# Performance work log

Hardware: AMD Instinct MI355X
Metric: run time of the kernel (lower is better)

Reference implementation:

```python
import jax, jax.numpy as jnp
import numpy as np

NUM_CAPSULE = 128   # must equal steps (seq_len) for the reshape in the original code
DIM_CAPSULE = 64
ROUTINGS = 3
EPS = 1e-7          # K.epsilon()


def pos_emb(x):
    """Sinusoidal position embedding added to x over its last two dims [..., S, D].
    Matches the Keras code: evens use sin(pos/10000^(2k/D)), odds use cos with the
    same frequency (odds-1 == 2k), interleaved via stack+reshape."""
    S, D = x.shape[-2], x.shape[-1]
    pos = jnp.arange(S, dtype=x.dtype)[:, None]                      # [S,1]
    inv_freq = 1.0 / jnp.power(10000.0, (2.0 * jnp.arange(D // 2, dtype=x.dtype)) / D)
    ang = pos * inv_freq[None, :]                                    # [S, D/2]
    pe = jnp.stack([jnp.sin(ang), jnp.cos(ang)], axis=-1).reshape(S, D)
    return x + pe


def squash(s):
    ss = jnp.sum(s * s, axis=-1, keepdims=True)
    scale = ss / (1.0 + ss) / jnp.sqrt(ss + EPS)
    return scale * s


def setup_inputs() -> dict:
    key = jax.random.key(0)
    k1, k2 = jax.random.split(key)
    B, steps, in_dim = 32, 128, 256
    u_vecs = jax.random.normal(k1, (B, steps, in_dim), dtype=jnp.float32)
    mask = jnp.ones((B, steps), dtype=jnp.float32)
    # glorot_uniform for capsule kernel (1, in_dim, dim_capsule)
    lim = float(np.sqrt(6.0 / (in_dim + DIM_CAPSULE)))
    W = jax.random.uniform(k2, (1, in_dim, DIM_CAPSULE), jnp.float32, -lim, lim)
    return {"u_vecs": u_vecs, "mask": mask, "W": W}


def reference(u_vecs, mask, W):
    B, steps, in_dim = u_vecs.shape
    N, D = NUM_CAPSULE, DIM_CAPSULE  # N == steps by construction
    # share_weights branch: tile W across steps, permute, add PE, flatten to a conv1d
    # kernel of width 1 -> a plain [in_dim, steps*D] projection matrix.
    tmp = jnp.transpose(jnp.broadcast_to(W, (steps, in_dim, D)), (1, 0, 2))  # [in_dim, steps, D]
    kernel = pos_emb(tmp).reshape(in_dim, steps * D)                          # [in_dim, steps*D]
    u_hat = jnp.einsum('bsi,io->bso', u_vecs, kernel)                         # [B, steps, steps*D]
    u_hat = pos_emb(u_hat)
    u_hat = u_hat.reshape(B, steps, N, D).transpose(0, 2, 1, 3)               # [B, N, In, D]
    b = jnp.zeros((B, N, steps), dtype=u_hat.dtype)                           # routing logits
    m = mask[:, None, :]                                                      # [B, 1, In]
    outputs = None
    for i in range(ROUTINGS):
        # softmax over the num_capsule axis (permute->softmax(-1)->permute in Keras)
        c = jax.nn.softmax(b, axis=1) * m                                     # [B, N, In]
        outputs = squash(jnp.einsum('bni,bnid->bnd', c, u_hat))               # [B, N, D]
        if i < ROUTINGS - 1:
            b = jnp.einsum('bnd,bnid->bni', outputs, u_hat)                   # agreement
    return outputs
```

## Files before the change

### kernel.cpp

```cpp
#include <hip/hip_runtime.h>
#include <math.h>

#define NB 32
#define NS 128
#define NI 256
#define NC 128
#define ND 64

#define L4 9.210340371976184f

__global__ __launch_bounds__(256) void k_prep(const float* __restrict__ u,
                                              const float* __restrict__ W,
                                              float* __restrict__ M,
                                              float* __restrict__ U,
                                              float* __restrict__ PE1) {
    int blk = blockIdx.x;
    int t = threadIdx.x;
    if (blk < 1024) {
        __shared__ float us[4][NI];
        int g = t >> 6, lane = t & 63;
        int row = blk * 4 + g;
        float4 v4 = ((const float4*)(u + (size_t)row * NI))[lane];
        ((float4*)us[g])[lane] = v4;
        float rs = v4.x + v4.y + v4.z + v4.w;
#pragma unroll
        for (int o = 32; o > 0; o >>= 1) rs += __shfl_xor(rs, o);
        if (lane == 0) U[row] = rs;
        float acc = 0.f;
#pragma unroll 8
        for (int i = 0; i < NI; ++i)
            acc = fmaf(us[g][i], W[i * ND + lane], acc);
        M[row * ND + lane] = acc;
    } else {
        int idx = (blk - 1024) * 256 + t;
        int n = idx >> 6, d = idx & 63;
        float ang = (float)n * __expf(-L4 * (float)(d >> 1) * (1.f / 32.f));
        float sv, cv;
        __sincosf(ang, &sv, &cv);
        PE1[idx] = (d & 1) ? cv : sv;
    }
}

__global__ __launch_bounds__(256, 4) void kR(const float* __restrict__ M,
                                             const float* __restrict__ U,
                                             const float* __restrict__ PE1,
                                             const float* __restrict__ cg,
                                             const float* __restrict__ mask,
                                             float* __restrict__ og,
                                             float* __restrict__ bl,
                                             int first, int last) {
    int bp = blockIdx.x;
    int n  = bp & 127;
    int b0 = (bp >> 7) * 2;
    int t  = threadIdx.x;

    __shared__ float  cs[NS][2];
    __shared__ float  Us[NS][2];
    __shared__ float4 redw[2][4][16];
    __shared__ float4 outs4[2][16];
    __shared__ float  tpar[2][2];
    __shared__ float  sc2[2][2];
    __shared__ float  red2[2][NS * 17];

    {
        int bh = t >> 7, s = t & 127;
        int b = b0 + bh;
        float uu = U[b * NS + s];
        float cv = first ? mask[b * NS + s] * (1.f / 128.f)
                         : cg[(b * NC + n) * NS + s];
        cs[s][bh] = cv;
        Us[s][bh] = uu;
        float p = cv * uu;
#pragma unroll
        for (int o = 32; o > 0; o >>= 1) p += __shfl_xor(p, o);
        if ((t & 63) == 0) tpar[bh][(t >> 6) & 1] = p;
    }

    float4 p14;
    if (t < 32) p14 = ((const float4*)PE1)[n * 16 + (t & 15)];

    int dq = t & 15, sq = t >> 4;
    int s0 = sq * 8;
    int k2 = n * 32 + dq * 2;
    float g0 = __expf(-L4 * (float)k2 * (1.f / 4096.f));
    float g1 = __expf(-L4 * (float)(k2 + 1) * (1.f / 4096.f));
    float sa = __sinf((float)s0 * g0), ca = __cosf((float)s0 * g0);
    float sb = __sinf((float)s0 * g1), cb = __cosf((float)s0 * g1);
    float sg0 = __sinf(g0), cg0 = __cosf(g0);
    float sg1 = __sinf(g1), cg1 = __cosf(g1);
    __syncthreads();

    float4 cc4[4];
    {
        const float4* csp = (const float4*)&cs[s0][0];
        cc4[0] = csp[0]; cc4[1] = csp[1]; cc4[2] = csp[2]; cc4[3] = csp[3];
    }

    const float4* M4a = (const float4*)(M + (size_t)(b0 * NS) * ND) + dq;
    const float4* M4b = M4a + NS * 16;
    float4 va[8], vb[8];
    float4 acc0 = make_float4(0.f, 0.f, 0.f, 0.f);
    float4 acc1 = make_float4(0.f, 0.f, 0.f, 0.f);
#pragma unroll
    for (int i = 0; i < 8; ++i) {
        int s = s0 + i;
        float4 m0 = M4a[s * 16];
        float4 m1 = M4b[s * 16];
        float2 cc = ((const float2*)cc4)[i];
        float4 u0, u1;
        u0.x = m0.x + sa; u0.y = m0.y + ca; u0.z = m0.z + sb; u0.w = m0.w + cb;
        u1.x = m1.x + sa; u1.y = m1.y + ca; u1.z = m1.z + sb; u1.w = m1.w + cb;
        va[i] = u0; vb[i] = u1;
        acc0.x = fmaf(cc.x, u0.x, acc0.x);
        acc0.y = fmaf(cc.x, u0.y, acc0.y);
        acc0.z = fmaf(cc.x, u0.z, acc0.z);
        acc0.w = fmaf(cc.x, u0.w, acc0.w);
        acc1.x = fmaf(cc.y, u1.x, acc1.x);
        acc1.y = fmaf(cc.y, u1.y, acc1.y);
        acc1.z = fmaf(cc.y, u1.z, acc1.z);
        acc1.w = fmaf(cc.y, u1.w, acc1.w);
        float nsa = fmaf(sa, cg0, ca * sg0);
        float nca = fmaf(ca, cg0, -sa * sg0);
        sa = nsa; ca = nca;
        float nsb = fmaf(sb, cg1, cb * sg1);
        float ncb = fmaf(cb, cg1, -sb * sg1);
        sb = nsb; cb = ncb;
    }
#pragma unroll
    for (int o = 16; o <= 32; o <<= 1) {
        acc0.x += __shfl_xor(acc0.x, o); acc0.y += __shfl_xor(acc0.y, o);
        acc0.z += __shfl_xor(acc0.z, o); acc0.w += __shfl_xor(acc0.w, o);
        acc1.x += __shfl_xor(acc1.x, o); acc1.y += __shfl_xor(acc1.y, o);
        acc1.z += __shfl_xor(acc1.z, o); acc1.w += __shfl_xor(acc1.w, o);
    }
    if ((t & 48) == 0) {
        int w = t >> 6;
        redw[0][w][dq] = acc0;
        redw[1][w][dq] = acc1;
    }
    __syncthreads();

    if (t < 32) {
        int bh = t >> 4, q = t & 15;
        float4 r0 = redw[bh][0][q], r1 = redw[bh][1][q];
        float4 r2 = redw[bh][2][q], r3 = redw[bh][3][q];
        float4 o;
        o.x = r0.x + r1.x + r2.x + r3.x;
        o.y = r0.y + r1.y + r2.y + r3.y;
        o.z = r0.z + r1.z + r2.z + r3.z;
        o.w = r0.w + r1.w + r2.w + r3.w;
        float T2 = tpar[bh][0] + tpar[bh][1];
        o.x = fmaf(p14.x, T2, o.x);
        o.y = fmaf(p14.y, T2, o.y);
        o.z = fmaf(p14.z, T2, o.z);
        o.w = fmaf(p14.w, T2, o.w);
        outs4[bh][q] = o;
        float ssq = o.x * o.x + o.y * o.y + o.z * o.z + o.w * o.w;
        float ppu = o.x * p14.x + o.y * p14.y + o.z * p14.z + o.w * p14.w;
#pragma unroll
        for (int o2 = 1; o2 <= 8; o2 <<= 1) {
            ssq += __shfl_xor(ssq, o2);
            ppu += __shfl_xor(ppu, o2);
        }
        if (q == 0) {
            sc2[bh][0] = ssq / (1.f + ssq) * rsqrtf(ssq + 1e-7f);
            sc2[bh][1] = ppu;
        }
    }
    __syncthreads();

    if (last) {
        if (t < 32) {
            int bh = t >> 4, q = t & 15;
            float sc = sc2[bh][0];
            float4 o = outs4[bh][q];
            o.x *= sc; o.y *= sc; o.z *= sc; o.w *= sc;
            ((float4*)og)[((b0 + bh) * NC + n) * 16 + q] = o;
        }
        return;
    }

    float4 oa = outs4[0][dq], ob = outs4[1][dq];
#pragma unroll
    for (int i = 0; i < 8; ++i) {
        int s = s0 + i;
        float4 v0 = va[i], v1 = vb[i];
        red2[0][s * 17 + dq] = v0.x * oa.x + v0.y * oa.y + v0.z * oa.z + v0.w * oa.w;
        red2[1][s * 17 + dq] = v1.x * ob.x + v1.y * ob.y + v1.z * ob.z + v1.w * ob.w;
    }
    __syncthreads();
    {
        int bh = t >> 7, s = t & 127;
        const float* r = &red2[bh][s * 17];
        float sum = 0.f;
#pragma unroll
        for (int q = 0; q < 16; ++q) sum += r[q];
        bl[((b0 + bh) * NC + n) * NS + s] =
            sc2[bh][0] * (sum + sc2[bh][1] * Us[s][bh]);
    }
}

__global__ __launch_bounds__(256) void kS(const float* __restrict__ bl,
                                          const float* __restrict__ mask,
                                          float* __restrict__ c) {
    int blk = blockIdx.x;
    int b = blk >> 3, s0 = (blk & 7) * 16;
    int t = threadIdx.x;

    __shared__ float tl[NC][17];
    __shared__ float pr[16][17];
    __shared__ float ps[16][17];
    __shared__ float itot[16], msk[16];

    if (t < 16) msk[t] = mask[b * NS + s0 + t];
#pragma unroll
    for (int i = 0; i < 8; ++i) {
        int idx = i * 256 + t;
        int n = idx >> 4, si = idx & 15;
        tl[n][si] = bl[(b * NC + n) * NS + s0 + si];
    }
    __syncthreads();

    int si = t & 15, ch = t >> 4;
    float mx = -1e30f;
#pragma unroll
    for (int j = 0; j < 8; ++j) mx = fmaxf(mx, tl[ch * 8 + j][si]);
    pr[ch][si] = mx;
    __syncthreads();

    mx = pr[0][si];
#pragma unroll
    for (int jc = 1; jc < 16; ++jc) mx = fmaxf(mx, pr[jc][si]);
    float sm = 0.f;
#pragma unroll
    for (int j = 0; j < 8; ++j) {
        float e = __expf(tl[ch * 8 + j][si] - mx);
        tl[ch * 8 + j][si] = e;
        sm += e;
    }
    ps[ch][si] = sm;
    __syncthreads();

    if (t < 16) {
        float tot = 0.f;
#pragma unroll
        for (int jc = 0; jc < 16; ++jc) tot += ps[jc][t];
        itot[t] = msk[t] / tot;
    }
    __syncthreads();

#pragma unroll
    for (int i = 0; i < 8; ++i) {
        int idx = i * 256 + t;
        int n = idx >> 4, sj = idx & 15;
        c[(b * NC + n) * NS + s0 + sj] = tl[n][sj] * itot[sj];
    }
}

extern "C" void kernel_launch(void* const* d_in, const int* in_sizes, int n_in,
                              void* d_out, int out_size, void* d_ws, size_t ws_size,
                              hipStream_t stream) {
    const float* u    = (const float*)d_in[0];
    const float* mask = (const float*)d_in[1];
    const float* W    = (const float*)d_in[2];
    float* out = (float*)d_out;

    float* ws  = (float*)d_ws;
    float* M   = ws;
    float* U   = M + NB * NS * ND;
    float* PE1 = U + NB * NS;
    float* c   = PE1 + NC * ND;
    float* bl  = c + NB * NC * NS;

    k_prep<<<1056, 256, 0, stream>>>(u, W, M, U, PE1);

    kR<<<2048, 256, 0, stream>>>(M, U, PE1, c, mask, out, bl, 1, 0);
    kS<<<NB * 8, 256, 0, stream>>>(bl, mask, c);
    kR<<<2048, 256, 0, stream>>>(M, U, PE1, c, mask, out, bl, 0, 0);
    kS<<<NB * 8, 256, 0, stream>>>(bl, mask, c);
    kR<<<2048, 256, 0, stream>>>(M, U, PE1, c, mask, out, bl, 0, 1);
}
```

Baseline: 103.8 us.

## Process two capsules per routing block and vectorize the projection in prep

The routing kernel now handles two capsules per block, so each M load feeds both capsules and the grid shrinks from 2048 to 1024 blocks. The goal is to halve global reads of M and the per-block setup cost. In exchange each thread holds twice as many register arrays and the block uses more shared memory, with launch bounds lowered to 2 blocks per SM. Separately, the prep kernel's projection splits the input dimension across lane groups, loads W as float4 and reduces partial sums with shuffles.

```diff
diff --git a/kernel.cpp b/kernel.cpp
--- a/kernel.cpp
+++ b/kernel.cpp
@@ -26,11 +26,28 @@
 #pragma unroll
         for (int o = 32; o > 0; o >>= 1) rs += __shfl_xor(rs, o);
         if (lane == 0) U[row] = rs;
-        float acc = 0.f;
+
+        int ih = lane >> 4, dq = lane & 15;
+        int base = ih * 64;
+        const float4* W4 = (const float4*)W;
+        float4 acc = make_float4(0.f, 0.f, 0.f, 0.f);
 #pragma unroll 8
-        for (int i = 0; i < NI; ++i)
-            acc = fmaf(us[g][i], W[i * ND + lane], acc);
-        M[row * ND + lane] = acc;
+        for (int ii = 0; ii < 64; ++ii) {
+            float uu = us[g][base + ii];
+            float4 w4 = W4[(base + ii) * 16 + dq];
+            acc.x = fmaf(uu, w4.x, acc.x);
+            acc.y = fmaf(uu, w4.y, acc.y);
+            acc.z = fmaf(uu, w4.z, acc.z);
+            acc.w = fmaf(uu, w4.w, acc.w);
+        }
+#pragma unroll
+        for (int o = 16; o <= 32; o <<= 1) {
+            acc.x += __shfl_xor(acc.x, o);
+            acc.y += __shfl_xor(acc.y, o);
+            acc.z += __shfl_xor(acc.z, o);
+            acc.w += __shfl_xor(acc.w, o);
+        }
+        if (ih == 0) ((float4*)M)[row * 16 + dq] = acc;
     } else {
         int idx = (blk - 1024) * 256 + t;
         int n = idx >> 6, d = idx & 63;
@@ -41,7 +58,7 @@
     }
 }
 
-__global__ __launch_bounds__(256, 4) void kR(const float* __restrict__ M,
+__global__ __launch_bounds__(256, 2) void kR(const float* __restrict__ M,
                                              const float* __restrict__ U,
                                              const float* __restrict__ PE1,
                                              const float* __restrict__ cg,
@@ -50,111 +67,148 @@
                                              float* __restrict__ bl,
                                              int first, int last) {
     int bp = blockIdx.x;
-    int n  = bp & 127;
-    int b0 = (bp >> 7) * 2;
+    int n0 = (bp & 63) * 2;
+    int b0 = (bp >> 6) * 2;
     int t  = threadIdx.x;
 
-    __shared__ float  cs[NS][2];
+    __shared__ float4 cs4[NS];
     __shared__ float  Us[NS][2];
-    __shared__ float4 redw[2][4][16];
-    __shared__ float4 outs4[2][16];
-    __shared__ float  tpar[2][2];
-    __shared__ float  sc2[2][2];
-    __shared__ float  red2[2][NS * 17];
+    __shared__ float4 redw[2][2][4][16];
+    __shared__ float4 outs4[2][2][16];
+    __shared__ float  tpar[2][2][2];
+    __shared__ float  sc2[2][2][2];
+    __shared__ float  red2[2][2][NS * 17];
 
     {
         int bh = t >> 7, s = t & 127;
         int b = b0 + bh;
         float uu = U[b * NS + s];
-        float cv = first ? mask[b * NS + s] * (1.f / 128.f)
-                         : cg[(b * NC + n) * NS + s];
-        cs[s][bh] = cv;
+        float cv0, cv1;
+        if (first) {
+            float mv = mask[b * NS + s] * (1.f / 128.f);
+            cv0 = mv; cv1 = mv;
+        } else {
+            cv0 = cg[(b * NC + n0) * NS + s];
+            cv1 = cg[(b * NC + n0 + 1) * NS + s];
+        }
+        ((float*)&cs4[s])[bh]     = cv0;
+        ((float*)&cs4[s])[2 + bh] = cv1;
         Us[s][bh] = uu;
-        float p = cv * uu;
-#pragma unroll
-        for (int o = 32; o > 0; o >>= 1) p += __shfl_xor(p, o);
-        if ((t & 63) == 0) tpar[bh][(t >> 6) & 1] = p;
+        float p0 = cv0 * uu, p1 = cv1 * uu;
+#pragma unroll
+        for (int o = 32; o > 0; o >>= 1) {
+            p0 += __shfl_xor(p0, o);
+            p1 += __shfl_xor(p1, o);
+        }
+        if ((t & 63) == 0) {
+            tpar[bh][0][(t >> 6) & 1] = p0;
+            tpar[bh][1][(t >> 6) & 1] = p1;
+        }
     }
 
     float4 p14;
-    if (t < 32) p14 = ((const float4*)PE1)[n * 16 + (t & 15)];
+    if (t < 64) {
+        int nh = (t >> 4) & 1, q = t & 15;
+        p14 = ((const float4*)PE1)[(n0 + nh) * 16 + q];
+    }
 
     int dq = t & 15, sq = t >> 4;
     int s0 = sq * 8;
-    int k2 = n * 32 + dq * 2;
-    float g0 = __expf(-L4 * (float)k2 * (1.f / 4096.f));
-    float g1 = __expf(-L4 * (float)(k2 + 1) * (1.f / 4096.f));
-    float sa = __sinf((float)s0 * g0), ca = __cosf((float)s0 * g0);
-    float sb = __sinf((float)s0 * g1), cb = __cosf((float)s0 * g1);
-    float sg0 = __sinf(g0), cg0 = __cosf(g0);
-    float sg1 = __sinf(g1), cg1 = __cosf(g1);
-    __syncthreads();
-
-    float4 cc4[4];
-    {
-        const float4* csp = (const float4*)&cs[s0][0];
-        cc4[0] = csp[0]; cc4[1] = csp[1]; cc4[2] = csp[2]; cc4[3] = csp[3];
-    }
+    int k20 = n0 * 32 + dq * 2;
+    int k21 = (n0 + 1) * 32 + dq * 2;
+    float g00 = __expf(-L4 * (float)k20 * (1.f / 4096.f));
+    float g01 = __expf(-L4 * (float)(k20 + 1) * (1.f / 4096.f));
+    float g10 = __expf(-L4 * (float)k21 * (1.f / 4096.f));
+    float g11 = __expf(-L4 * (float)(k21 + 1) * (1.f / 4096.f));
+    float sa0, ca0, sb0, cb0, sa1, ca1, sb1, cb1;
+    __sincosf((float)s0 * g00, &sa0, &ca0);
+    __sincosf((float)s0 * g01, &sb0, &cb0);
+    __sincosf((float)s0 * g10, &sa1, &ca1);
+    __sincosf((float)s0 * g11, &sb1, &cb1);
+    float sg00, cg00, sg01, cg01, sg10, cg10, sg11, cg11;
+    __sincosf(g00, &sg00, &cg00);
+    __sincosf(g01, &sg01, &cg01);
+    __sincosf(g10, &sg10, &cg10);
+    __sincosf(g11, &sg11, &cg11);
+    __syncthreads();
 
     const float4* M4a = (const float4*)(M + (size_t)(b0 * NS) * ND) + dq;
     const float4* M4b = M4a + NS * 16;
-    float4 va[8], vb[8];
-    float4 acc0 = make_float4(0.f, 0.f, 0.f, 0.f);
-    float4 acc1 = make_float4(0.f, 0.f, 0.f, 0.f);
+    float4 vA0[8], vB0[8], vA1[8], vB1[8];
+    float4 accA0 = make_float4(0.f, 0.f, 0.f, 0.f);
+    float4 accB0 = make_float4(0.f, 0.f, 0.f, 0.f);
+    float4 accA1 = make_float4(0.f, 0.f, 0.f, 0.f);
+    float4 accB1 = make_float4(0.f, 0.f, 0.f, 0.f);
 #pragma unroll
     for (int i = 0; i < 8; ++i) {
         int s = s0 + i;
         float4 m0 = M4a[s * 16];
         float4 m1 = M4b[s * 16];
-        float2 cc = ((const float2*)cc4)[i];
-        float4 u0, u1;
-        u0.x = m0.x + sa; u0.y = m0.y + ca; u0.z = m0.z + sb; u0.w = m0.w + cb;
-        u1.x = m1.x + sa; u1.y = m1.y + ca; u1.z = m1.z + sb; u1.w = m1.w + cb;
-        va[i] = u0; vb[i] = u1;
-        acc0.x = fmaf(cc.x, u0.x, acc0.x);
-        acc0.y = fmaf(cc.x, u0.y, acc0.y);
-        acc0.z = fmaf(cc.x, u0.z, acc0.z);
-        acc0.w = fmaf(cc.x, u0.w, acc0.w);
-        acc1.x = fmaf(cc.y, u1.x, acc1.x);
-        acc1.y = fmaf(cc.y, u1.y, acc1.y);
-        acc1.z = fmaf(cc.y, u1.z, acc1.z);
-        acc1.w = fmaf(cc.y, u1.w, acc1.w);
-        float nsa = fmaf(sa, cg0, ca * sg0);
-        float nca = fmaf(ca, cg0, -sa * sg0);
-        sa = nsa; ca = nca;
-        float nsb = fmaf(sb, cg1, cb * sg1);
-        float ncb = fmaf(cb, cg1, -sb * sg1);
-        sb = nsb; cb = ncb;
+        float4 cc = cs4[s];
+        float4 u00, u10, u01, u11;
+        u00.x = m0.x + sa0; u00.y = m0.y + ca0; u00.z = m0.z + sb0; u00.w = m0.w + cb0;
+        u10.x = m1.x + sa0; u10.y = m1.y + ca0; u10.z = m1.z + sb0; u10.w = m1.w + cb0;
+        u01.x = m0.x + sa1; u01.y = m0.y + ca1; u01.z = m0.z + sb1; u01.w = m0.w + cb1;
+        u11.x = m1.x + sa1; u11.y = m1.y + ca1; u11.z = m1.z + sb1; u11.w = m1.w + cb1;
+        vA0[i] = u00; vB0[i] = u10; vA1[i] = u01; vB1[i] = u11;
+        accA0.x = fmaf(cc.x, u00.x, accA0.x);
+        accA0.y = fmaf(cc.x, u00.y, accA0.y);
+        accA0.z = fmaf(cc.x, u00.z, accA0.z);
+        accA0.w = fmaf(cc.x, u00.w, accA0.w);
+        accB0.x = fmaf(cc.y, u10.x, accB0.x);
+        accB0.y = fmaf(cc.y, u10.y, accB0.y);
+        accB0.z = fmaf(cc.y, u10.z, accB0.z);
+        accB0.w = fmaf(cc.y, u10.w, accB0.w);
+        accA1.x = fmaf(cc.z, u01.x, accA1.x);
+        accA1.y = fmaf(cc.z, u01.y, accA1.y);
+        accA1.z = fmaf(cc.z, u01.z, accA1.z);
+        accA1.w = fmaf(cc.z, u01.w, accA1.w);
+        accB1.x = fmaf(cc.w, u11.x, accB1.x);
+        accB1.y = fmaf(cc.w, u11.y, accB1.y);
+        accB1.z = fmaf(cc.w, u11.z, accB1.z);
+        accB1.w = fmaf(cc.w, u11.w, accB1.w);
+        float ns, nc;
+        ns = fmaf(sa0, cg00, ca0 * sg00); nc = fmaf(ca0, cg00, -sa0 * sg00); sa0 = ns; ca0 = nc;
+        ns = fmaf(sb0, cg01, cb0 * sg01); nc = fmaf(cb0, cg01, -sb0 * sg01); sb0 = ns; cb0 = nc;
+        ns = fmaf(sa1, cg10, ca1 * sg10); nc = fmaf(ca1, cg10, -sa1 * sg10); sa1 = ns; ca1 = nc;
+        ns = fmaf(sb1, cg11, cb1 * sg11); nc = fmaf(cb1, cg11, -sb1 * sg11); sb1 = ns; cb1 = nc;
     }
 #pragma unroll
     for (int o = 16; o <= 32; o <<= 1) {
-        acc0.x += __shfl_xor(acc0.x, o); acc0.y += __shfl_xor(acc0.y, o);
-        acc0.z += __shfl_xor(acc0.z, o); acc0.w += __shfl_xor(acc0.w, o);
-        acc1.x += __shfl_xor(acc1.x, o); acc1.y += __shfl_xor(acc1.y, o);
-        acc1.z += __shfl_xor(acc1.z, o); acc1.w += __shfl_xor(acc1.w, o);
+        accA0.x += __shfl_xor(accA0.x, o); accA0.y += __shfl_xor(accA0.y, o);
+        accA0.z += __shfl_xor(accA0.z, o); accA0.w += __shfl_xor(accA0.w, o);
+        accB0.x += __shfl_xor(accB0.x, o); accB0.y += __shfl_xor(accB0.y, o);
+        accB0.z += __shfl_xor(accB0.z, o); accB0.w += __shfl_xor(accB0.w, o);
+        accA1.x += __shfl_xor(accA1.x, o); accA1.y += __shfl_xor(accA1.y, o);
+        accA1.z += __shfl_xor(accA1.z, o); accA1.w += __shfl_xor(accA1.w, o);
+        accB1.x += __shfl_xor(accB1.x, o); accB1.y += __shfl_xor(accB1.y, o);
+        accB1.z += __shfl_xor(accB1.z, o); accB1.w += __shfl_xor(accB1.w, o);
     }
     if ((t & 48) == 0) {
         int w = t >> 6;
-        redw[0][w][dq] = acc0;
-        redw[1][w][dq] = acc1;
-    }
-    __syncthreads();
-
-    if (t < 32) {
-        int bh = t >> 4, q = t & 15;
-        float4 r0 = redw[bh][0][q], r1 = redw[bh][1][q];
-        float4 r2 = redw[bh][2][q], r3 = redw[bh][3][q];
+        redw[0][0][w][dq] = accA0;
+        redw[1][0][w][dq] = accB0;
+        redw[0][1][w][dq] = accA1;
+        redw[1][1][w][dq] = accB1;
+    }
+    __syncthreads();
+
+    if (t < 64) {
+        int combo = t >> 4, q = t & 15;
+        int bh = combo >> 1, nh = combo & 1;
+        float4 r0 = redw[bh][nh][0][q], r1 = redw[bh][nh][1][q];
+        float4 r2 = redw[bh][nh][2][q], r3 = redw[bh][nh][3][q];
         float4 o;
         o.x = r0.x + r1.x + r2.x + r3.x;
         o.y = r0.y + r1.y + r2.y + r3.y;
         o.z = r0.z + r1.z + r2.z + r3.z;
         o.w = r0.w + r1.w + r2.w + r3.w;
-        float T2 = tpar[bh][0] + tpar[bh][1];
+        float T2 = tpar[bh][nh][0] + tpar[bh][nh][1];
         o.x = fmaf(p14.x, T2, o.x);
         o.y = fmaf(p14.y, T2, o.y);
         o.z = fmaf(p14.z, T2, o.z);
         o.w = fmaf(p14.w, T2, o.w);
-        outs4[bh][q] = o;
+        outs4[bh][nh][q] = o;
         float ssq = o.x * o.x + o.y * o.y + o.z * o.z + o.w * o.w;
         float ppu = o.x * p14.x + o.y * p14.y + o.z * p14.z + o.w * p14.w;
 #pragma unroll
@@ -163,40 +217,52 @@
             ppu += __shfl_xor(ppu, o2);
         }
         if (q == 0) {
-            sc2[bh][0] = ssq / (1.f + ssq) * rsqrtf(ssq + 1e-7f);
-            sc2[bh][1] = ppu;
+            sc2[bh][nh][0] = ssq / (1.f + ssq) * rsqrtf(ssq + 1e-7f);
+            sc2[bh][nh][1] = ppu;
         }
     }
     __syncthreads();
 
     if (last) {
-        if (t < 32) {
-            int bh = t >> 4, q = t & 15;
-            float sc = sc2[bh][0];
-            float4 o = outs4[bh][q];
+        if (t < 64) {
+            int combo = t >> 4, q = t & 15;
+            int bh = combo >> 1, nh = combo & 1;
+            float sc = sc2[bh][nh][0];
+            float4 o = outs4[bh][nh][q];
             o.x *= sc; o.y *= sc; o.z *= sc; o.w *= sc;
-            ((float4*)og)[((b0 + bh) * NC + n) * 16 + q] = o;
+            ((float4*)og)[((b0 + bh) * NC + n0 + nh) * 16 + q] = o;
         }
         return;
     }
 
-    float4 oa = outs4[0][dq], ob = outs4[1][dq];
+    float4 oA0 = outs4[0][0][dq], oB0 = outs4[1][0][dq];
+    float4 oA1 = outs4[0][1][dq], oB1 = outs4[1][1][dq];
 #pragma unroll
     for (int i = 0; i < 8; ++i) {
         int s = s0 + i;
-        float4 v0 = va[i], v1 = vb[i];
-        red2[0][s * 17 + dq] = v0.x * oa.x + v0.y * oa.y + v0.z * oa.z + v0.w * oa.w;
-        red2[1][s * 17 + dq] = v1.x * ob.x + v1.y * ob.y + v1.z * ob.z + v1.w * ob.w;
+        float4 v;
+        v = vA0[i];
+        red2[0][0][s * 17 + dq] = v.x * oA0.x + v.y * oA0.y + v.z * oA0.z + v.w * oA0.w;
+        v = vB0[i];
+        red2[1][0][s * 17 + dq] = v.x * oB0.x + v.y * oB0.y + v.z * oB0.z + v.w * oB0.w;
+        v = vA1[i];
+        red2[0][1][s * 17 + dq] = v.x * oA1.x + v.y * oA1.y + v.z * oA1.z + v.w * oA1.w;
+        v = vB1[i];
+        red2[1][1][s * 17 + dq] = v.x * oB1.x + v.y * oB1.y + v.z * oB1.z + v.w * oB1.w;
     }
     __syncthreads();
     {
         int bh = t >> 7, s = t & 127;
-        const float* r = &red2[bh][s * 17];
-        float sum = 0.f;
-#pragma unroll
-        for (int q = 0; q < 16; ++q) sum += r[q];
-        bl[((b0 + bh) * NC + n) * NS + s] =
-            sc2[bh][0] * (sum + sc2[bh][1] * Us[s][bh]);
+        float uu = Us[s][bh];
+#pragma unroll
+        for (int nh = 0; nh < 2; ++nh) {
+            const float* r = &red2[bh][nh][s * 17];
+            float sum = 0.f;
+#pragma unroll
+            for (int q = 0; q < 16; ++q) sum += r[q];
+            bl[((b0 + bh) * NC + n0 + nh) * NS + s] =
+                sc2[bh][nh][0] * (sum + sc2[bh][nh][1] * uu);
+        }
     }
 }
 
@@ -274,9 +340,9 @@
 
     k_prep<<<1056, 256, 0, stream>>>(u, W, M, U, PE1);
 
-    kR<<<2048, 256, 0, stream>>>(M, U, PE1, c, mask, out, bl, 1, 0);
+    kR<<<1024, 256, 0, stream>>>(M, U, PE1, c, mask, out, bl, 1, 0);
     kS<<<NB * 8, 256, 0, stream>>>(bl, mask, c);
-    kR<<<2048, 256, 0, stream>>>(M, U, PE1, c, mask, out, bl, 0, 0);
+    kR<<<1024, 256, 0, stream>>>(M, U, PE1, c, mask, out, bl, 0, 0);
     kS<<<NB * 8, 256, 0, stream>>>(bl, mask, c);
-    kR<<<2048, 256, 0, stream>>>(M, U, PE1, c, mask, out, bl, 0, 1);
+    kR<<<1024, 256, 0, stream>>>(M, U, PE1, c, mask, out, bl, 0, 1);
 }
```

Result: slower. 112.7 us (+8.6%).

## Tile prep GEMM with 16 rows per block and W staged in shared memory

Applied to the files above, without the earlier changes.

The prep kernel now gives each block 16 input rows instead of 4, stages W in shared memory in two 128-row halves, and gives each thread a 2x2 register tile (two rows, two output columns). The intent is to cut the redundant global reads of W across the 1024 former blocks and raise arithmetic intensity per load. The cost is fewer blocks (256 instead of 1024) and about 48KB of LDS per block, which lowers occupancy and parallelism for this stage.

```diff
diff --git a/kernel.cpp b/kernel.cpp
--- a/kernel.cpp
+++ b/kernel.cpp
@@ -16,23 +16,62 @@
                                               float* __restrict__ PE1) {
     int blk = blockIdx.x;
     int t = threadIdx.x;
-    if (blk < 1024) {
-        __shared__ float us[4][NI];
-        int g = t >> 6, lane = t & 63;
-        int row = blk * 4 + g;
-        float4 v4 = ((const float4*)(u + (size_t)row * NI))[lane];
-        ((float4*)us[g])[lane] = v4;
-        float rs = v4.x + v4.y + v4.z + v4.w;
-#pragma unroll
-        for (int o = 32; o > 0; o >>= 1) rs += __shfl_xor(rs, o);
-        if (lane == 0) U[row] = rs;
-        float acc = 0.f;
+    if (blk < 256) {
+        __shared__ float us[16][NI];
+        __shared__ float ws[128 * ND];
+        int r0 = blk * 16;
+
+        {
+            const float4* u4 = (const float4*)(u + (size_t)r0 * NI);
+            float4* us4 = (float4*)us;
+            float up = 0.f;
+#pragma unroll
+            for (int j = 0; j < 4; ++j) {
+                int fi = t * 4 + j;
+                float4 v = u4[fi];
+                us4[fi] = v;
+                up += v.x + v.y + v.z + v.w;
+            }
+#pragma unroll
+            for (int o = 1; o <= 8; o <<= 1) up += __shfl_xor(up, o);
+            if ((t & 15) == 0) U[r0 + (t >> 4)] = up;
+        }
+
+        int lane = t & 63, w = t >> 6;
+        int dp = lane & 31;
+        int rh = lane >> 5;
+        int rA = w * 4 + rh * 2, rB = rA + 1;
+        float2 accA = make_float2(0.f, 0.f), accB = make_float2(0.f, 0.f);
+        const float4* W4 = (const float4*)W;
+
+        for (int p = 0; p < 2; ++p) {
+            __syncthreads();
+            {
+                float4* ws4 = (float4*)ws;
+#pragma unroll
+                for (int j = 0; j < 8; ++j) {
+                    int fi = t + 256 * j;
+                    ws4[fi] = W4[p * 2048 + fi];
+                }
+            }
+            __syncthreads();
+            int ibase = p * 128;
 #pragma unroll 8
-        for (int i = 0; i < NI; ++i)
-            acc = fmaf(us[g][i], W[i * ND + lane], acc);
-        M[row * ND + lane] = acc;
+            for (int ii = 0; ii < 128; ++ii) {
+                float2 wv = *(const float2*)&ws[ii * ND + dp * 2];
+                float ua = us[rA][ibase + ii];
+                float ub = us[rB][ibase + ii];
+                accA.x = fmaf(ua, wv.x, accA.x);
+                accA.y = fmaf(ua, wv.y, accA.y);
+                accB.x = fmaf(ub, wv.x, accB.x);
+                accB.y = fmaf(ub, wv.y, accB.y);
+            }
+        }
+        float2* M2 = (float2*)M;
+        M2[(size_t)(r0 + rA) * 32 + dp] = accA;
+        M2[(size_t)(r0 + rB) * 32 + dp] = accB;
     } else {
-        int idx = (blk - 1024) * 256 + t;
+        int idx = (blk - 256) * 256 + t;
         int n = idx >> 6, d = idx & 63;
         float ang = (float)n * __expf(-L4 * (float)(d >> 1) * (1.f / 32.f));
         float sv, cv;
@@ -272,7 +311,7 @@
     float* c   = PE1 + NC * ND;
     float* bl  = c + NB * NC * NS;
 
-    k_prep<<<1056, 256, 0, stream>>>(u, W, M, U, PE1);
+    k_prep<<<288, 256, 0, stream>>>(u, W, M, U, PE1);
 
     kR<<<2048, 256, 0, stream>>>(M, U, PE1, c, mask, out, bl, 1, 0);
     kS<<<NB * 8, 256, 0, stream>>>(bl, mask, c);
```

Measured after the change: 99.61 us. 4.0% less time.
